# Kernel optimization log

Measured on AMD Instinct MI355X. Metric: run time of the kernel, lower is better.

## Reference

```python
import jax, jax.numpy as jnp
import numpy as np

D_MODEL = 256
D_HEAD = 64
N_HEAD = 8


def setup_inputs() -> dict:
    key = jax.random.key(0)
    ks = jax.random.split(key, 8)
    b, h, w = 32, 64, 64
    dk = D_HEAD * N_HEAD
    s = 1.0 / np.sqrt(D_MODEL)
    x = jax.random.normal(ks[0], (b, D_MODEL, h, w), dtype=jnp.float32)
    query = jax.random.normal(ks[1], (b, D_MODEL), dtype=jnp.float32)
    Wkv = jax.random.uniform(ks[2], (2 * dk, D_MODEL), jnp.float32, -s, s)
    bkv = jax.random.uniform(ks[3], (2 * dk,), jnp.float32, -s, s)
    Wq = jax.random.uniform(ks[4], (dk, D_MODEL), jnp.float32, -s, s)
    bq = jax.random.uniform(ks[5], (dk,), jnp.float32, -s, s)
    sf = 1.0 / np.sqrt(dk)
    Wfc = jax.random.uniform(ks[6], (D_MODEL, dk), jnp.float32, -sf, sf)
    bfc = jax.random.uniform(ks[7], (D_MODEL,), jnp.float32, -sf, sf)
    return {"x": x, "query": query, "Wkv": Wkv, "bkv": bkv, "Wq": Wq, "bq": bq, "Wfc": Wfc, "bfc": bfc}


def reference(x, query, Wkv, bkv, Wq, bq, Wfc, bfc):
    b, c, h, w = x.shape
    t = h * w
    scale = 1.0 / np.sqrt(D_HEAD).astype(np.float32)
    # 1x1 conv == per-pixel linear: (b, 2*n*d, t)
    kv = jnp.einsum('bchw,oc->bohw', x, Wkv).reshape(b, 2 * N_HEAD, D_HEAD, t)
    kv = kv + bkv.reshape(1, 2 * N_HEAD, D_HEAD, 1)
    k, v = kv[:, :N_HEAD], kv[:, N_HEAD:]  # each (b, n, d, t)
    q = (query @ Wq.T + bq).reshape(b, N_HEAD, D_HEAD)
    logits = jnp.einsum('bnd,bndj->bnj', q, k) * scale
    attn = jax.nn.softmax(logits, axis=2)
    out = jnp.einsum('bnj,bndj->bnd', attn, v).reshape(b, N_HEAD * D_HEAD)
    return jax.nn.relu(out @ Wfc.T + bfc)
```

## Files before the change

### kernel.cpp

```cpp
#include <hip/hip_runtime.h>
#include <hip/hip_bf16.h>

#define B_     32
#define C_     256
#define T_     4096
#define NH_    8
#define DH_    64

__global__ __launch_bounds__(256) void k_prep(
    const float* __restrict__ query, const float* __restrict__ Wkv,
    const float* __restrict__ bkv, const float* __restrict__ Wq,
    const float* __restrict__ bq, float* __restrict__ qWt,
    float* __restrict__ qb) {
  const int n = blockIdx.x;
  const int b = blockIdx.y;
  const int t = threadIdx.x;
  __shared__ float qrow_s[C_];
  __shared__ float psum[4 * 64];
  __shared__ float qsh[64];
  __shared__ float pb_s[64];

  qrow_s[t] = query[(size_t)b * C_ + t];
  __syncthreads();

  {
    const int d = t & 63, ch = t >> 6;
    const float* wrow = Wq + (size_t)(n * DH_ + d) * C_ + ch * 64;
    const float* qr = qrow_s + ch * 64;
    float s = 0.f;
    #pragma unroll
    for (int c = 0; c < 64; c += 4) {
      float4 w = *(const float4*)(wrow + c);
      s += w.x * qr[c] + w.y * qr[c + 1] + w.z * qr[c + 2] + w.w * qr[c + 3];
    }
    psum[ch * 64 + d] = s;
  }
  __syncthreads();
  if (t < 64)
    qsh[t] = bq[n * DH_ + t] + psum[t] + psum[64 + t] + psum[128 + t] + psum[192 + t];
  __syncthreads();

  const float scale = 0.125f;
  {
    const float* wk = Wkv + (size_t)(n * DH_) * C_ + t;
    float acc = 0.f;
    #pragma unroll 8
    for (int dd = 0; dd < DH_; ++dd) acc += qsh[dd] * wk[(size_t)dd * C_];
    qWt[((size_t)b * C_ + t) * NH_ + n] = acc * scale;
  }
  if (t < 64) pb_s[t] = qsh[t] * bkv[n * DH_ + t];
  __syncthreads();
  if (t == 0) {
    float s = 0.f;
    #pragma unroll 8
    for (int dd = 0; dd < 64; ++dd) s += pb_s[dd];
    qb[b * NH_ + n] = s * scale;
  }
}

__global__ __launch_bounds__(128) void k_logits(
    const float* __restrict__ x, const float* __restrict__ qWt,
    const float* __restrict__ qbv, float* __restrict__ lgpart) {
  const int half = blockIdx.y;
  const int b = blockIdx.z;
  const int t = threadIdx.x;
  const int j = blockIdx.x * 512 + t * 4;
  __shared__ float qws[128 * NH_];

  {
    const float* src = qWt + (size_t)b * (C_ * NH_) + half * 1024;
    *(float4*)(qws + t * 8)     = *(const float4*)(src + t * 8);
    *(float4*)(qws + t * 8 + 4) = *(const float4*)(src + t * 8 + 4);
  }
  __syncthreads();

  const float* xb = x + ((size_t)b * C_ + half * 128) * T_ + j;
  const float* qb = qbv + b * NH_;

  float4 acc[NH_];
  #pragma unroll
  for (int n = 0; n < NH_; ++n) {
    const float init = half ? 0.f : qb[n];
    acc[n].x = init; acc[n].y = init; acc[n].z = init; acc[n].w = init;
  }

#define FMA8_(W, A) { A.x += (W) * xv4.x; A.y += (W) * xv4.y; \
                      A.z += (W) * xv4.z; A.w += (W) * xv4.w; }
  for (int c0 = 0; c0 < 128; c0 += 8) {
    float4 xv[8];
    #pragma unroll
    for (int cc = 0; cc < 8; ++cc)
      xv[cc] = *(const float4*)(xb + (size_t)(c0 + cc) * T_);
    #pragma unroll
    for (int cc = 0; cc < 8; ++cc) {
      const float4 w0 = *(const float4*)(qws + (c0 + cc) * 8);
      const float4 w1 = *(const float4*)(qws + (c0 + cc) * 8 + 4);
      const float4 xv4 = xv[cc];
      FMA8_(w0.x, acc[0]); FMA8_(w0.y, acc[1]);
      FMA8_(w0.z, acc[2]); FMA8_(w0.w, acc[3]);
      FMA8_(w1.x, acc[4]); FMA8_(w1.y, acc[5]);
      FMA8_(w1.z, acc[6]); FMA8_(w1.w, acc[7]);
    }
  }
#undef FMA8_

  float* lg = lgpart + (((size_t)half * B_ + b) * NH_) * T_ + j;
  #pragma unroll
  for (int n = 0; n < NH_; ++n)
    *(float4*)(lg + (size_t)n * T_) = acc[n];
}

__global__ __launch_bounds__(256) void k_softmax(
    const float* __restrict__ lgpart, float* __restrict__ attn) {
  const size_t row = blockIdx.x;
  const float* p0 = lgpart + row * T_;
  const float* p1 = lgpart + ((size_t)B_ * NH_ + row) * T_;
  float* pa = attn + row * T_;
  const int t = threadIdx.x;
  float4 v[4];
  #pragma unroll
  for (int i = 0; i < 4; ++i) {
    float4 a = *(const float4*)(p0 + t * 4 + i * 1024);
    float4 c = *(const float4*)(p1 + t * 4 + i * 1024);
    v[i].x = a.x + c.x; v[i].y = a.y + c.y; v[i].z = a.z + c.z; v[i].w = a.w + c.w;
  }

  float m = -3.4e38f;
  #pragma unroll
  for (int i = 0; i < 4; ++i)
    m = fmaxf(m, fmaxf(fmaxf(v[i].x, v[i].y), fmaxf(v[i].z, v[i].w)));
  #pragma unroll
  for (int o = 32; o >= 1; o >>= 1) m = fmaxf(m, __shfl_xor(m, o));
  __shared__ float sm[4];
  if ((t & 63) == 0) sm[t >> 6] = m;
  __syncthreads();
  m = fmaxf(fmaxf(sm[0], sm[1]), fmaxf(sm[2], sm[3]));

  float s = 0.f;
  #pragma unroll
  for (int i = 0; i < 4; ++i) {
    v[i].x = expf(v[i].x - m); v[i].y = expf(v[i].y - m);
    v[i].z = expf(v[i].z - m); v[i].w = expf(v[i].w - m);
    s += v[i].x + v[i].y + v[i].z + v[i].w;
  }
  #pragma unroll
  for (int o = 32; o >= 1; o >>= 1) s += __shfl_xor(s, o);
  __shared__ float ss[4];
  if ((t & 63) == 0) ss[t >> 6] = s;
  __syncthreads();
  s = ss[0] + ss[1] + ss[2] + ss[3];
  const float inv = 1.0f / s;

  #pragma unroll
  for (int i = 0; i < 4; ++i) {
    v[i].x *= inv; v[i].y *= inv; v[i].z *= inv; v[i].w *= inv;
    *(float4*)(pa + t * 4 + i * 1024) = v[i];
  }
}

#define BJ_  256
#define BJS_ 32
#define XPITCH_ 33
__global__ __launch_bounds__(256) void k_xattn(
    const float* __restrict__ x, const float* __restrict__ attn,
    float* __restrict__ part) {
  const int jt = blockIdx.x;
  const int b  = blockIdx.y;
  const int j0 = jt * BJ_;
  const int t  = threadIdx.x;
  __shared__ float xs[2][C_ * XPITCH_];

  const float* xb = x + (size_t)b * C_ * T_;
  const float* ab = attn + (size_t)b * NH_ * T_ + j0;

  float acc[NH_];
  #pragma unroll
  for (int n = 0; n < NH_; ++n) acc[n] = 0.f;

  const int cr = t >> 3;
  const int jc = (t & 7) * 4;

  {
    float4 v[8];
    #pragma unroll
    for (int p = 0; p < 8; ++p)
      v[p] = *(const float4*)(xb + (size_t)(cr + p * 32) * T_ + j0 + jc);
    #pragma unroll
    for (int p = 0; p < 8; ++p) {
      float* dst = &xs[0][(cr + p * 32) * XPITCH_ + jc];
      dst[0] = v[p].x; dst[1] = v[p].y; dst[2] = v[p].z; dst[3] = v[p].w;
    }
  }
  __syncthreads();

  for (int sIt = 0; sIt < BJ_ / BJS_; ++sIt) {
    const int buf = sIt & 1;
    float4 v[8];
    if (sIt < BJ_ / BJS_ - 1) {
      const int js = (sIt + 1) * BJS_;
      #pragma unroll
      for (int p = 0; p < 8; ++p)
        v[p] = *(const float4*)(xb + (size_t)(cr + p * 32) * T_ + j0 + js + jc);
    }

    const float* xr = &xs[buf][t * XPITCH_];
    const int jsc = sIt * BJS_;
    #pragma unroll
    for (int jg = 0; jg < BJS_ / 4; ++jg) {
      const int j4 = jg * 4;
      const float x0 = xr[j4 + 0], x1 = xr[j4 + 1];
      const float x2 = xr[j4 + 2], x3 = xr[j4 + 3];
      #pragma unroll
      for (int n = 0; n < NH_; ++n) {
        const float4 a = *(const float4*)(ab + (size_t)n * T_ + jsc + j4);
        acc[n] += a.x * x0 + a.y * x1 + a.z * x2 + a.w * x3;
      }
    }

    if (sIt < BJ_ / BJS_ - 1) {
      #pragma unroll
      for (int p = 0; p < 8; ++p) {
        float* dst = &xs[buf ^ 1][(cr + p * 32) * XPITCH_ + jc];
        dst[0] = v[p].x; dst[1] = v[p].y; dst[2] = v[p].z; dst[3] = v[p].w;
      }
    }
    __syncthreads();
  }

  float* pb = part + ((size_t)b * 16 + jt) * (NH_ * C_);
  #pragma unroll
  for (int n = 0; n < NH_; ++n) pb[n * C_ + t] = acc[n];
}

__global__ __launch_bounds__(256) void k_outv(
    const float* __restrict__ part, const float* __restrict__ Wkv,
    const float* __restrict__ bkv, float* __restrict__ outvG) {
  __shared__ float xa_s[4 * C_];
  const int hb = blockIdx.x;
  const int b  = blockIdx.y;
  const int t  = threadIdx.x;

  const float* pb = part + (size_t)b * 16 * (NH_ * C_) + hb * (4 * C_);
  #pragma unroll
  for (int r = 0; r < 4; ++r) {
    const int idx = r * 256 + t;
    float s = 0.f;
    #pragma unroll
    for (int jt = 0; jt < 16; ++jt) s += pb[(size_t)jt * (NH_ * C_) + idx];
    xa_s[idx] = s;
  }
  __syncthreads();

  const int o = hb * 256 + t;
  const float* wrow = Wkv + (size_t)(512 + o) * C_;
  const float* xa = &xa_s[(t >> 6) * C_];
  float s = bkv[512 + o];
  #pragma unroll 8
  for (int c = 0; c < C_; c += 4) {
    float4 w = *(const float4*)(wrow + c);
    s += w.x * xa[c] + w.y * xa[c + 1] + w.z * xa[c + 2] + w.w * xa[c + 3];
  }
  outvG[(size_t)b * 512 + o] = s;
}

__global__ __launch_bounds__(256) void k_fc(
    const float* __restrict__ outvG, const float* __restrict__ Wfc,
    const float* __restrict__ bfc, float* __restrict__ out) {
  __shared__ float ov[512];
  const int hx = blockIdx.x;
  const int b  = blockIdx.y;
  const int t  = threadIdx.x;
  ov[t] = outvG[(size_t)b * 512 + t];
  ov[256 + t] = outvG[(size_t)b * 512 + 256 + t];
  __syncthreads();

  const int m    = hx * 128 + (t >> 1);
  const int half = t & 1;
  const float* wrow = Wfc + (size_t)m * 512 + half * 256;
  const float* o = ov + half * 256;
  float s = half ? 0.f : bfc[m];
  #pragma unroll 8
  for (int c = 0; c < 256; c += 4) {
    float4 w = *(const float4*)(wrow + c);
    s += w.x * o[c] + w.y * o[c + 1] + w.z * o[c + 2] + w.w * o[c + 3];
  }
  s += __shfl_xor(s, 1);
  if (!half) out[(size_t)b * 256 + m] = fmaxf(s, 0.f);
}

extern "C" void kernel_launch(void* const* d_in, const int* in_sizes, int n_in,
                              void* d_out, int out_size, void* d_ws, size_t ws_size,
                              hipStream_t stream) {
  const float* x     = (const float*)d_in[0];
  const float* query = (const float*)d_in[1];
  const float* Wkv   = (const float*)d_in[2];
  const float* bkv   = (const float*)d_in[3];
  const float* Wq    = (const float*)d_in[4];
  const float* bq    = (const float*)d_in[5];
  const float* Wfc   = (const float*)d_in[6];
  const float* bfc   = (const float*)d_in[7];
  float* out = (float*)d_out;
  float* ws  = (float*)d_ws;

  float* qWt    = ws;
  float* qb     = ws + 65536;
  float* lgpart = ws + 66048;
  float* attn   = ws + 2163200;
  float* part   = ws + 3211776;
  float* outvG  = ws + 4260352;

  k_prep   <<<dim3(NH_, B_),   256, 0, stream>>>(query, Wkv, bkv, Wq, bq, qWt, qb);
  k_logits <<<dim3(8, 2, B_),  128, 0, stream>>>(x, qWt, qb, lgpart);
  k_softmax<<<B_ * NH_,        256, 0, stream>>>(lgpart, attn);
  k_xattn  <<<dim3(16, B_),    256, 0, stream>>>(x, attn, part);
  k_outv   <<<dim3(2, B_),     256, 0, stream>>>(part, Wkv, bkv, outvG);
  k_fc     <<<dim3(2, B_),     256, 0, stream>>>(outvG, Wfc, bfc, out);
}
```

Before: 279.0 us.

## Fuse value projection and FC into one tail kernel; single-buffer x tile

Merges the value-projection and output FC kernels into one 512-thread kernel per batch, keeping the intermediate in shared memory instead of global workspace and removing one launch. The x-times-attention kernel drops its double-buffered shared-memory prefetch for a single buffer loaded synchronously each step. This halves shared memory per block, which may allow more resident blocks. In exchange, the overlap between global loads and compute is lost, and the tail runs with fewer blocks.

```diff
diff --git a/kernel.cpp b/kernel.cpp
--- a/kernel.cpp
+++ b/kernel.cpp
@@ -168,7 +168,7 @@
   const int b  = blockIdx.y;
   const int j0 = jt * BJ_;
   const int t  = threadIdx.x;
-  __shared__ float xs[2][C_ * XPITCH_];
+  __shared__ float xs[C_ * XPITCH_];
 
   const float* xb = x + (size_t)b * C_ * T_;
   const float* ab = attn + (size_t)b * NH_ * T_ + j0;
@@ -180,31 +180,18 @@
   const int cr = t >> 3;
   const int jc = (t & 7) * 4;
 
-  {
-    float4 v[8];
-    #pragma unroll
-    for (int p = 0; p < 8; ++p)
-      v[p] = *(const float4*)(xb + (size_t)(cr + p * 32) * T_ + j0 + jc);
+  for (int sIt = 0; sIt < BJ_ / BJS_; ++sIt) {
+    const int js = sIt * BJS_;
+    __syncthreads();
     #pragma unroll
     for (int p = 0; p < 8; ++p) {
-      float* dst = &xs[0][(cr + p * 32) * XPITCH_ + jc];
-      dst[0] = v[p].x; dst[1] = v[p].y; dst[2] = v[p].z; dst[3] = v[p].w;
-    }
-  }
-  __syncthreads();
-
-  for (int sIt = 0; sIt < BJ_ / BJS_; ++sIt) {
-    const int buf = sIt & 1;
-    float4 v[8];
-    if (sIt < BJ_ / BJS_ - 1) {
-      const int js = (sIt + 1) * BJS_;
-      #pragma unroll
-      for (int p = 0; p < 8; ++p)
-        v[p] = *(const float4*)(xb + (size_t)(cr + p * 32) * T_ + j0 + js + jc);
-    }
-
-    const float* xr = &xs[buf][t * XPITCH_];
-    const int jsc = sIt * BJS_;
+      const int c = cr + p * 32;
+      float4 vv = *(const float4*)(xb + (size_t)c * T_ + j0 + js + jc);
+      float* dst = &xs[c * XPITCH_ + jc];
+      dst[0] = vv.x; dst[1] = vv.y; dst[2] = vv.z; dst[3] = vv.w;
+    }
+    __syncthreads();
+    const float* xr = &xs[t * XPITCH_];
     #pragma unroll
     for (int jg = 0; jg < BJS_ / 4; ++jg) {
       const int j4 = jg * 4;
@@ -212,19 +199,10 @@
       const float x2 = xr[j4 + 2], x3 = xr[j4 + 3];
       #pragma unroll
       for (int n = 0; n < NH_; ++n) {
-        const float4 a = *(const float4*)(ab + (size_t)n * T_ + jsc + j4);
+        const float4 a = *(const float4*)(ab + (size_t)n * T_ + js + j4);
         acc[n] += a.x * x0 + a.y * x1 + a.z * x2 + a.w * x3;
       }
     }
-
-    if (sIt < BJ_ / BJS_ - 1) {
-      #pragma unroll
-      for (int p = 0; p < 8; ++p) {
-        float* dst = &xs[buf ^ 1][(cr + p * 32) * XPITCH_ + jc];
-        dst[0] = v[p].x; dst[1] = v[p].y; dst[2] = v[p].z; dst[3] = v[p].w;
-      }
-    }
-    __syncthreads();
   }
 
   float* pb = part + ((size_t)b * 16 + jt) * (NH_ * C_);
@@ -232,18 +210,19 @@
   for (int n = 0; n < NH_; ++n) pb[n * C_ + t] = acc[n];
 }
 
-__global__ __launch_bounds__(256) void k_outv(
+__global__ __launch_bounds__(512) void k_tail(
     const float* __restrict__ part, const float* __restrict__ Wkv,
-    const float* __restrict__ bkv, float* __restrict__ outvG) {
-  __shared__ float xa_s[4 * C_];
-  const int hb = blockIdx.x;
-  const int b  = blockIdx.y;
-  const int t  = threadIdx.x;
-
-  const float* pb = part + (size_t)b * 16 * (NH_ * C_) + hb * (4 * C_);
+    const float* __restrict__ bkv, const float* __restrict__ Wfc,
+    const float* __restrict__ bfc, float* __restrict__ out) {
+  __shared__ float xa_s[NH_ * C_];
+  __shared__ float ov[512];
+  const int b = blockIdx.x;
+  const int t = threadIdx.x;
+
+  const float* pb = part + (size_t)b * 16 * (NH_ * C_);
   #pragma unroll
   for (int r = 0; r < 4; ++r) {
-    const int idx = r * 256 + t;
+    const int idx = r * 512 + t;
     float s = 0.f;
     #pragma unroll
     for (int jt = 0; jt < 16; ++jt) s += pb[(size_t)jt * (NH_ * C_) + idx];
@@ -251,41 +230,31 @@
   }
   __syncthreads();
 
-  const int o = hb * 256 + t;
-  const float* wrow = Wkv + (size_t)(512 + o) * C_;
-  const float* xa = &xa_s[(t >> 6) * C_];
-  float s = bkv[512 + o];
-  #pragma unroll 8
-  for (int c = 0; c < C_; c += 4) {
-    float4 w = *(const float4*)(wrow + c);
-    s += w.x * xa[c] + w.y * xa[c + 1] + w.z * xa[c + 2] + w.w * xa[c + 3];
-  }
-  outvG[(size_t)b * 512 + o] = s;
-}
-
-__global__ __launch_bounds__(256) void k_fc(
-    const float* __restrict__ outvG, const float* __restrict__ Wfc,
-    const float* __restrict__ bfc, float* __restrict__ out) {
-  __shared__ float ov[512];
-  const int hx = blockIdx.x;
-  const int b  = blockIdx.y;
-  const int t  = threadIdx.x;
-  ov[t] = outvG[(size_t)b * 512 + t];
-  ov[256 + t] = outvG[(size_t)b * 512 + 256 + t];
-  __syncthreads();
-
-  const int m    = hx * 128 + (t >> 1);
-  const int half = t & 1;
-  const float* wrow = Wfc + (size_t)m * 512 + half * 256;
-  const float* o = ov + half * 256;
-  float s = half ? 0.f : bfc[m];
-  #pragma unroll 8
-  for (int c = 0; c < 256; c += 4) {
-    float4 w = *(const float4*)(wrow + c);
-    s += w.x * o[c] + w.y * o[c + 1] + w.z * o[c + 2] + w.w * o[c + 3];
-  }
-  s += __shfl_xor(s, 1);
-  if (!half) out[(size_t)b * 256 + m] = fmaxf(s, 0.f);
+  {
+    const int o = t;
+    const float* wrow = Wkv + (size_t)(512 + o) * C_;
+    const float* xa = &xa_s[(o >> 6) * C_];
+    float s = bkv[512 + o];
+    #pragma unroll 8
+    for (int c = 0; c < C_; c += 4) {
+      float4 w = *(const float4*)(wrow + c);
+      s += w.x * xa[c] + w.y * xa[c + 1] + w.z * xa[c + 2] + w.w * xa[c + 3];
+    }
+    ov[o] = s;
+  }
+  __syncthreads();
+
+  if (t < 256) {
+    const int m = t;
+    const float* wrow = Wfc + (size_t)m * 512;
+    float s = bfc[m];
+    #pragma unroll 8
+    for (int o = 0; o < 512; o += 4) {
+      float4 w = *(const float4*)(wrow + o);
+      s += w.x * ov[o] + w.y * ov[o + 1] + w.z * ov[o + 2] + w.w * ov[o + 3];
+    }
+    out[(size_t)b * 256 + m] = fmaxf(s, 0.f);
+  }
 }
 
 extern "C" void kernel_launch(void* const* d_in, const int* in_sizes, int n_in,
@@ -307,12 +276,10 @@
   float* lgpart = ws + 66048;
   float* attn   = ws + 2163200;
   float* part   = ws + 3211776;
-  float* outvG  = ws + 4260352;
 
   k_prep   <<<dim3(NH_, B_),   256, 0, stream>>>(query, Wkv, bkv, Wq, bq, qWt, qb);
   k_logits <<<dim3(8, 2, B_),  128, 0, stream>>>(x, qWt, qb, lgpart);
   k_softmax<<<B_ * NH_,        256, 0, stream>>>(lgpart, attn);
   k_xattn  <<<dim3(16, B_),    256, 0, stream>>>(x, attn, part);
-  k_outv   <<<dim3(2, B_),     256, 0, stream>>>(part, Wkv, bkv, outvG);
-  k_fc     <<<dim3(2, B_),     256, 0, stream>>>(outvG, Wfc, bfc, out);
-}
+  k_tail   <<<B_,              512, 0, stream>>>(part, Wkv, bkv, Wfc, bfc, out);
+}
```

New measurement: 303.7 us. 1.09x slower.
